# Kernel optimization log

Hardware: AMD Instinct MI355X
Metric: run time of the kernel (lower is better)

## Reference

```python
import jax, jax.numpy as jnp
import numpy as np

N_GRAPHS = 100
NODES_PER_GRAPH = 1000
N = N_GRAPHS * NODES_PER_GRAPH
DEG = 16
E = N * DEG
IN_FEATS = 64
HIDDEN = 128
READOUT_DIM = HIDDEN // 2
SLOPE = 0.01
EPS = 1e-5


def leaky(x):
    return jnp.where(x >= 0, x, SLOPE * x)


def _kaiming(k, shape):
    # torch kaiming_uniform_, fan_in mode, leaky_relu gain
    fan_in = shape[0]
    gain = np.sqrt(2.0 / (1.0 + SLOPE ** 2))
    bound = gain * np.sqrt(3.0 / fan_in)
    return jax.random.uniform(k, shape, jnp.float32, -bound, bound)


def setup_inputs() -> dict:
    key = jax.random.key(0)
    ks = jax.random.split(key, 16)
    node_feats = jax.random.normal(ks[0], (N, IN_FEATS), jnp.float32)
    # within-graph random edges (batched graph of equal-sized components)
    src_local = jax.random.randint(ks[1], (E,), 0, NODES_PER_GRAPH)
    dst_local = jax.random.randint(ks[2], (E,), 0, NODES_PER_GRAPH)
    edge_graph = jnp.repeat(jnp.arange(N_GRAPHS, dtype=jnp.int32), E // N_GRAPHS)
    src = (edge_graph * NODES_PER_GRAPH + src_local).astype(jnp.int32)
    dst = (edge_graph * NODES_PER_GRAPH + dst_local).astype(jnp.int32)
    edge_weights = jax.random.uniform(ks[3], (E,), jnp.float32)
    node_graph = jnp.repeat(jnp.arange(N_GRAPHS, dtype=jnp.int32), NODES_PER_GRAPH)
    return {
        "node_feats": node_feats,
        "edge_weights": edge_weights,
        "W1": _kaiming(ks[4], (IN_FEATS, HIDDEN)),
        "W2": _kaiming(ks[5], (HIDDEN, HIDDEN)),
        "gn1_alpha": jnp.ones((HIDDEN,), jnp.float32),
        "gn1_gamma": jnp.ones((HIDDEN,), jnp.float32),
        "gn1_beta": jnp.zeros((HIDDEN,), jnp.float32),
        "gn2_alpha": jnp.ones((HIDDEN,), jnp.float32),
        "gn2_gamma": jnp.ones((HIDDEN,), jnp.float32),
        "gn2_beta": jnp.zeros((HIDDEN,), jnp.float32),
        "r1_w1": _kaiming(ks[6], (HIDDEN, HIDDEN)),
        "r1_b1": jnp.zeros((HIDDEN,), jnp.float32),
        "r1_w2": _kaiming(ks[7], (HIDDEN, READOUT_DIM)),
        "r1_b2": jnp.zeros((READOUT_DIM,), jnp.float32),
        "r2_w1": _kaiming(ks[8], (HIDDEN, HIDDEN)),
        "r2_b1": jnp.zeros((HIDDEN,), jnp.float32),
        "r2_w2": _kaiming(ks[9], (HIDDEN, READOUT_DIM)),
        "r2_b2": jnp.zeros((READOUT_DIM,), jnp.float32),
        "src": src,
        "dst": dst,
        "node_graph": node_graph,
    }


def _graph_conv(x, W, src, dst, ew, out_isqrt, in_isqrt):
    # DGL GraphConv norm='both', no bias: D_in^{-1/2} A_w D_out^{-1/2} X W
    h = (x * out_isqrt[:, None]) @ W                 # [N, out]
    m = h[src] * ew[:, None]                         # [E, out] gather + edge weight
    agg = jax.ops.segment_sum(m, dst, num_segments=N)  # scatter-add
    return agg * in_isqrt[:, None]


def _graph_norm(x, alpha, gamma, beta, node_graph, inv_cnt):
    mean = jax.ops.segment_sum(x, node_graph, num_segments=N_GRAPHS) * inv_cnt
    sub = x - alpha * mean[node_graph]
    var = jax.ops.segment_sum(sub * sub, node_graph, num_segments=N_GRAPHS) * inv_cnt
    return gamma * sub / jnp.sqrt(var[node_graph] + EPS) + beta


def _readout(x, w1, b1, w2, b2, node_graph, inv_cnt):
    # deep-sets style universal readout: rho(mean(phi(h_v)))
    h = leaky(x @ w1 + b1)
    pooled = jax.ops.segment_sum(h, node_graph, num_segments=N_GRAPHS) * inv_cnt
    return leaky(pooled @ w2 + b2)


def reference(node_feats, edge_weights, W1, W2,
              gn1_alpha, gn1_gamma, gn1_beta,
              gn2_alpha, gn2_gamma, gn2_beta,
              r1_w1, r1_b1, r1_w2, r1_b2,
              r2_w1, r2_b1, r2_w2, r2_b2,
              src, dst, node_graph):
    ones_e = jnp.ones((E,), jnp.float32)
    out_deg = jnp.clip(jax.ops.segment_sum(ones_e, src, num_segments=N), 1.0)
    in_deg = jnp.clip(jax.ops.segment_sum(ones_e, dst, num_segments=N), 1.0)
    out_isqrt = jax.lax.rsqrt(out_deg)
    in_isqrt = jax.lax.rsqrt(in_deg)
    inv_cnt = 1.0 / NODES_PER_GRAPH

    h = _graph_conv(node_feats, W1, src, dst, edge_weights, out_isqrt, in_isqrt)
    h = leaky(_graph_norm(h, gn1_alpha, gn1_gamma, gn1_beta, node_graph, inv_cnt))
    # dropout is identity in eval mode
    r1 = _readout(h, r1_w1, r1_b1, r1_w2, r1_b2, node_graph, inv_cnt)
    m1 = jax.ops.segment_sum(h, node_graph, num_segments=N_GRAPHS) * inv_cnt

    h = _graph_conv(h, W2, src, dst, edge_weights, out_isqrt, in_isqrt)
    h = leaky(_graph_norm(h, gn2_alpha, gn2_gamma, gn2_beta, node_graph, inv_cnt))
    r2 = _readout(h, r2_w1, r2_b1, r2_w2, r2_b2, node_graph, inv_cnt)
    m2 = jax.ops.segment_sum(h, node_graph, num_segments=N_GRAPHS) * inv_cnt

    readout = jnp.concatenate([r1, m1, r2, m2], axis=1)  # [G, 2*H + 2*H/2] = [100, 384]
    return leaky(readout)
```

## Files before the change

### kernel.cpp

```cpp
#include <hip/hip_runtime.h>
#include <cstddef>
#include <cstdint>

#define NG   100
#define NPG  1000
#define NN   (NG * NPG)
#define NE   (NN * 16)
#define EPG  (NE / NG)
#define CSRG 20000
#define FIN  64
#define HID  128
#define RD   64
#define SLOPE 0.01f
#define EPSV  1e-5f
#define NSTRIP 250
#define GSN   40

using short8 = __attribute__((ext_vector_type(8))) short;
using f32x4  = __attribute__((ext_vector_type(4))) float;
typedef unsigned short u16;

__device__ __forceinline__ float leaky(float x) { return x >= 0.f ? x : SLOPE * x; }

__device__ __forceinline__ u16 f2bf(float f) {
  union { float f; unsigned u; } v; v.f = f;
  return (u16)((v.u + 0x7fffu + ((v.u >> 16) & 1u)) >> 16);
}
__device__ __forceinline__ float bf2f(u16 u) {
  union { unsigned u; float f; } v; v.u = ((unsigned)u) << 16;
  return v.f;
}

__device__ __forceinline__ bool swz(int b, int per_g, int& g, int& part) {
  const int xcd = b & 7;
  const int slot = b >> 3;
  g = xcd + 8 * (slot / per_g);
  part = slot % per_g;
  return g < NG;
}

__global__ __launch_bounds__(256) void wt_k(const float* __restrict__ W1,
                                            const float* __restrict__ W2,
                                            const float* __restrict__ R1,
                                            const float* __restrict__ R2,
                                            u16* __restrict__ Wt1,
                                            u16* __restrict__ Wt2,
                                            u16* __restrict__ Rt1,
                                            u16* __restrict__ Rt2) {
  const int idx = blockIdx.x * 256 + threadIdx.x;
  if (idx < FIN * HID) {
    const int n = idx >> 6, k = idx & 63;
    Wt1[idx] = f2bf(W1[k * HID + n]);
  } else {
    const int j = idx - FIN * HID;
    const int m = j >> 14, r = j & 16383;
    const int n = r >> 7, k = r & 127;
    const float* s = (m == 0) ? W2 : (m == 1) ? R1 : R2;
    u16* d = (m == 0) ? Wt2 : (m == 1) ? Rt1 : Rt2;
    d[r] = f2bf(s[k * HID + n]);
  }
}

__global__ __launch_bounds__(1024) void build_k(const int* __restrict__ src,
                                                const int* __restrict__ dst,
                                                const float* __restrict__ ew,
                                                int* __restrict__ cin_,
                                                int* __restrict__ cout_,
                                                int* __restrict__ offs,
                                                unsigned* __restrict__ csr) {
  __shared__ int hin[NPG];
  __shared__ int hout[NPG];
  __shared__ int cur[NPG];
  __shared__ int wtot[16];
  int g, part;
  if (!swz(blockIdx.x, 1, g, part)) return;
  const int t = threadIdx.x;
  const int lane = t & 63, wave = t >> 6;
  const int nb = g * NPG, eb = g * EPG;
  if (t < NPG) { hin[t] = 0; hout[t] = 0; }
  __syncthreads();
  for (int e = t; e < EPG; e += 1024) {
    atomicAdd(&hout[src[eb + e] - nb], 1);
    atomicAdd(&hin[dst[eb + e] - nb], 1);
  }
  __syncthreads();
  int v[4], vr[4];
  int loc = 0;
#pragma unroll
  for (int k = 0; k < 4; ++k) {
    const int idx = t * 4 + k;
    v[k] = (idx < NPG) ? hin[idx] : 0;
    vr[k] = (v[k] + 3) & ~3;
    loc += vr[k];
  }
  int incl = loc;
#pragma unroll
  for (int d = 1; d < 64; d <<= 1) {
    const int x = __shfl_up(incl, d);
    if (lane >= d) incl += x;
  }
  if (lane == 63) wtot[wave] = incl;
  if (t < NPG) { cin_[nb + t] = hin[t]; cout_[nb + t] = hout[t]; }
  __syncthreads();
  int wexc = 0;
  for (int i = 0; i < wave; ++i) wexc += wtot[i];
  int run = g * CSRG + wexc + (incl - loc);
#pragma unroll
  for (int k = 0; k < 4; ++k) {
    const int idx = t * 4 + k;
    if (idx < NPG) {
      offs[nb + idx] = run;
      cur[idx] = run;
      run += vr[k];
    }
  }
  __syncthreads();
  for (int e = t; e < EPG; e += 1024) {
    const int d = dst[eb + e] - nb;
    const int pos = atomicAdd(&cur[d], 1);
    csr[pos] = ((unsigned)(src[eb + e] - nb) << 16) | (unsigned)f2bf(ew[eb + e]);
  }
}

__global__ __launch_bounds__(256) void gemm1_k(const float* __restrict__ X,
                                               const u16* __restrict__ Wt,
                                               const int* __restrict__ cout_,
                                               u16* __restrict__ Y) {
  __shared__ u16 Xl[64 * FIN];
  __shared__ u16 Wl[HID * FIN];
  const int tid = threadIdx.x;
  const int wave = tid >> 6, lane = tid & 63, l15 = lane & 15, quad = lane >> 4;
  int g, part;
  if (!swz(blockIdx.x, 4, g, part)) return;
  const int base = g * NPG + part * NSTRIP;

  for (int i = tid; i < HID * (FIN / 8); i += 256) {
    const int n = i >> 3, c = i & 7;
    const short8 w = *(const short8*)(Wt + n * FIN + c * 8);
    *(short8*)&Wl[n * FIN + ((c ^ (n & 7)) << 3)] = w;
  }
  for (int pass = 0; pass < 4; ++pass) {
    __syncthreads();
    for (int i = tid; i < 64 * (FIN / 4); i += 256) {
      const int r = i >> 4;
      const int kq = i & 15;
      const int rowi = pass * 64 + r;
      ushort4 u = make_ushort4(0, 0, 0, 0);
      if (rowi < NSTRIP) {
        const float4 x = *(const float4*)(X + (size_t)(base + rowi) * FIN + kq * 4);
        u.x = f2bf(x.x); u.y = f2bf(x.y); u.z = f2bf(x.z); u.w = f2bf(x.w);
      }
      const int c = kq >> 1, half = kq & 1;
      *(ushort4*)&Xl[r * FIN + (((c ^ (r & 7)) << 3) | (half << 2))] = u;
    }
    __syncthreads();
    short8 a[2];
    const int arow = wave * 16 + l15;
#pragma unroll
    for (int kt = 0; kt < 2; ++kt)
      a[kt] = *(const short8*)&Xl[arow * FIN + (((kt * 4 + quad) ^ (l15 & 7)) << 3)];
    float sc[4];
    int rows[4];
#pragma unroll
    for (int r = 0; r < 4; ++r) {
      rows[r] = pass * 64 + wave * 16 + quad * 4 + r;
      sc[r] = (rows[r] < NSTRIP) ? rsqrtf(fmaxf((float)cout_[base + rows[r]], 1.0f)) : 0.f;
    }
#pragma unroll
    for (int ct = 0; ct < 8; ++ct) {
      f32x4 acc = {0.f, 0.f, 0.f, 0.f};
      const int brow = ct * 16 + l15;
#pragma unroll
      for (int kt = 0; kt < 2; ++kt) {
        const short8 b = *(const short8*)&Wl[brow * FIN + (((kt * 4 + quad) ^ (l15 & 7)) << 3)];
        acc = __builtin_amdgcn_mfma_f32_16x16x32_bf16(a[kt], b, acc, 0, 0, 0);
      }
      const int n = ct * 16 + l15;
#pragma unroll
      for (int r = 0; r < 4; ++r)
        if (rows[r] < NSTRIP) Y[(size_t)(base + rows[r]) * HID + n] = f2bf(acc[r] * sc[r]);
    }
  }
}

__global__ __launch_bounds__(256) void gemm_norm_k(const u16* __restrict__ Xb,
                                                   const u16* __restrict__ Wt,
                                                   const float* __restrict__ An,
                                                   const float* __restrict__ Bn,
                                                   const int* __restrict__ cout_,
                                                   u16* __restrict__ Y) {
  __shared__ u16 Xl[64 * HID];
  __shared__ u16 Wl[HID * HID];
  const int tid = threadIdx.x;
  const int wave = tid >> 6, lane = tid & 63, l15 = lane & 15, quad = lane >> 4;
  int g, part;
  if (!swz(blockIdx.x, 4, g, part)) return;
  const int base = g * NPG + part * NSTRIP;

  for (int i = tid; i < HID * (HID / 8); i += 256) {
    const int n = i >> 4, c = i & 15;
    const short8 w = *(const short8*)(Wt + n * HID + c * 8);
    *(short8*)&Wl[n * HID + ((c ^ (n & 15)) << 3)] = w;
  }
  for (int pass = 0; pass < 4; ++pass) {
    __syncthreads();
    for (int i = tid; i < 64 * 16; i += 256) {
      const int r = i >> 4;
      const int c8 = i & 15;
      const int rowi = pass * 64 + r;
      short8 o = {0, 0, 0, 0, 0, 0, 0, 0};
      if (rowi < NSTRIP) {
        const int node = base + rowi;
        const short8 xs = *(const short8*)(Xb + (size_t)node * HID + c8 * 8);
        const float4 Aa = *(const float4*)(An + (size_t)g * HID + c8 * 8);
        const float4 Ab = *(const float4*)(An + (size_t)g * HID + c8 * 8 + 4);
        const float4 Ba = *(const float4*)(Bn + (size_t)g * HID + c8 * 8);
        const float4 Bb = *(const float4*)(Bn + (size_t)g * HID + c8 * 8 + 4);
        const float Av[8] = {Aa.x, Aa.y, Aa.z, Aa.w, Ab.x, Ab.y, Ab.z, Ab.w};
        const float Bv[8] = {Ba.x, Ba.y, Ba.z, Ba.w, Bb.x, Bb.y, Bb.z, Bb.w};
#pragma unroll
        for (int j = 0; j < 8; ++j)
          o[j] = (short)f2bf(leaky(fmaf(Av[j], bf2f((u16)xs[j]), Bv[j])));
      }
      *(short8*)&Xl[r * HID + ((c8 ^ (r & 15)) << 3)] = o;
    }
    __syncthreads();
    short8 a[4];
    const int arow = wave * 16 + l15;
#pragma unroll
    for (int kt = 0; kt < 4; ++kt)
      a[kt] = *(const short8*)&Xl[arow * HID + (((kt * 4 + quad) ^ l15) << 3)];
    float sc[4];
    int rows[4];
#pragma unroll
    for (int r = 0; r < 4; ++r) {
      rows[r] = pass * 64 + wave * 16 + quad * 4 + r;
      sc[r] = (rows[r] < NSTRIP) ? rsqrtf(fmaxf((float)cout_[base + rows[r]], 1.0f)) : 0.f;
    }
#pragma unroll
    for (int ct = 0; ct < 8; ++ct) {
      f32x4 acc = {0.f, 0.f, 0.f, 0.f};
      const int brow = ct * 16 + l15;
#pragma unroll
      for (int kt = 0; kt < 4; ++kt) {
        const short8 b = *(const short8*)&Wl[brow * HID + (((kt * 4 + quad) ^ l15) << 3)];
        acc = __builtin_amdgcn_mfma_f32_16x16x32_bf16(a[kt], b, acc, 0, 0, 0);
      }
      const int n = ct * 16 + l15;
#pragma unroll
      for (int r = 0; r < 4; ++r)
        if (rows[r] < NSTRIP) Y[(size_t)(base + rows[r]) * HID + n] = f2bf(acc[r] * sc[r]);
    }
  }
}

__global__ __launch_bounds__(256) void phi_pool_k(const u16* __restrict__ Xb,
                                                  const float* __restrict__ An,
                                                  const float* __restrict__ Bn,
                                                  const u16* __restrict__ Wt,
                                                  const float* __restrict__ b1,
                                                  float* __restrict__ phi_sum,
                                                  float* __restrict__ h_sum) {
  __shared__ u16 Xl[64 * HID];
  __shared__ u16 Wl[HID * HID];
  __shared__ float red[16][HID];
  __shared__ float hred[16][HID];
  const int tid = threadIdx.x;
  const int wave = tid >> 6, lane = tid & 63, l15 = lane & 15, quad = lane >> 4;
  int g, part;
  if (!swz(blockIdx.x, 4, g, part)) return;
  const int base = g * NPG + part * NSTRIP;

  for (int i = tid; i < HID * (HID / 8); i += 256) {
    const int n = i >> 4, c = i & 15;
    const short8 w = *(const short8*)(Wt + n * HID + c * 8);
    *(short8*)&Wl[n * HID + ((c ^ (n & 15)) << 3)] = w;
  }
  float bcol[8];
#pragma unroll
  for (int ct = 0; ct < 8; ++ct) bcol[ct] = b1[ct * 16 + l15];

  float pooled[8] = {0.f, 0.f, 0.f, 0.f, 0.f, 0.f, 0.f, 0.f};
  float hp[8] = {0.f, 0.f, 0.f, 0.f, 0.f, 0.f, 0.f, 0.f};

  for (int pass = 0; pass < 4; ++pass) {
    __syncthreads();
    for (int i = tid; i < 64 * 16; i += 256) {
      const int r = i >> 4;
      const int c8 = i & 15;
      const int rowi = pass * 64 + r;
      short8 o = {0, 0, 0, 0, 0, 0, 0, 0};
      if (rowi < NSTRIP) {
        const int node = base + rowi;
        const short8 xs = *(const short8*)(Xb + (size_t)node * HID + c8 * 8);
        const float4 Aa = *(const float4*)(An + (size_t)g * HID + c8 * 8);
        const float4 Ab = *(const float4*)(An + (size_t)g * HID + c8 * 8 + 4);
        const float4 Ba = *(const float4*)(Bn + (size_t)g * HID + c8 * 8);
        const float4 Bb = *(const float4*)(Bn + (size_t)g * HID + c8 * 8 + 4);
        const float Av[8] = {Aa.x, Aa.y, Aa.z, Aa.w, Ab.x, Ab.y, Ab.z, Ab.w};
        const float Bv[8] = {Ba.x, Ba.y, Ba.z, Ba.w, Bb.x, Bb.y, Bb.z, Bb.w};
#pragma unroll
        for (int j = 0; j < 8; ++j) {
          const float xn = leaky(fmaf(Av[j], bf2f((u16)xs[j]), Bv[j]));
          hp[j] += xn;
          o[j] = (short)f2bf(xn);
        }
      }
      *(short8*)&Xl[r * HID + ((c8 ^ (r & 15)) << 3)] = o;
    }
    __syncthreads();
    short8 a[4];
    const int arow = wave * 16 + l15;
#pragma unroll
    for (int kt = 0; kt < 4; ++kt)
      a[kt] = *(const short8*)&Xl[arow * HID + (((kt * 4 + quad) ^ l15) << 3)];
#pragma unroll
    for (int ct = 0; ct < 8; ++ct) {
      f32x4 acc = {0.f, 0.f, 0.f, 0.f};
      const int brow = ct * 16 + l15;
#pragma unroll
      for (int kt = 0; kt < 4; ++kt) {
        const short8 b = *(const short8*)&Wl[brow * HID + (((kt * 4 + quad) ^ l15) << 3)];
        acc = __builtin_amdgcn_mfma_f32_16x16x32_bf16(a[kt], b, acc, 0, 0, 0);
      }
#pragma unroll
      for (int r = 0; r < 4; ++r) {
        const int rowi = pass * 64 + wave * 16 + quad * 4 + r;
        if (rowi < NSTRIP) pooled[ct] += leaky(acc[r] + bcol[ct]);
      }
    }
  }
  const int qi = wave * 4 + quad;
#pragma unroll
  for (int ct = 0; ct < 8; ++ct) red[qi][ct * 16 + l15] = pooled[ct];
#pragma unroll
  for (int j = 0; j < 8; ++j) hred[tid >> 4][(tid & 15) * 8 + j] = hp[j];
  __syncthreads();
  if (tid < HID) {
    float s = 0.f;
#pragma unroll
    for (int q = 0; q < 16; ++q) s += red[q][tid];
    unsafeAtomicAdd(&phi_sum[g * HID + tid], s);
  } else {
    const int t = tid - HID;
    float s = 0.f;
#pragma unroll
    for (int rr = 0; rr < 16; ++rr) s += hred[rr][t];
    unsafeAtomicAdd(&h_sum[g * HID + t], s);
  }
}

__global__ __launch_bounds__(256) void gather_k(const u16* __restrict__ H,
                                                const unsigned* __restrict__ csr,
                                                const int* __restrict__ offs,
                                                const int* __restrict__ cin_,
                                                u16* __restrict__ AGG,
                                                float* __restrict__ sx,
                                                float* __restrict__ sq) {
  __shared__ float redx[4][HID];
  __shared__ float redq[4][HID];
  const int wave = threadIdx.x >> 6;
  const int lane = threadIdx.x & 63;
  int g, part;
  if (!swz(blockIdx.x, 25, g, part)) return;
  const int nb = g * NPG;
  const int base = nb + part * GSN;
  const int loff = lane * 2;
  const u16* __restrict__ Hg = H + (size_t)nb * HID;

  float sxa = 0.f, sxb = 0.f, sqa = 0.f, sqb = 0.f;
  for (int i = 0; i < 5; ++i) {
    const int nA = base + wave + i * 4;
    const int nB = nA + GSN / 2;
    const int nuA = __builtin_amdgcn_readfirstlane(nA);
    const int nuB = __builtin_amdgcn_readfirstlane(nB);
    const int offA = __builtin_amdgcn_readfirstlane(offs[nuA]);
    const int cntA = __builtin_amdgcn_readfirstlane(cin_[nuA]);
    const int offB = __builtin_amdgcn_readfirstlane(offs[nuB]);
    const int cntB = __builtin_amdgcn_readfirstlane(cin_[nuB]);
    const float isqA = rsqrtf(fmaxf((float)cntA, 1.0f));
    const float isqB = rsqrtf(fmaxf((float)cntB, 1.0f));
    const uint4* __restrict__ pA =
        (const uint4*)__builtin_assume_aligned(csr + offA, 16);
    const uint4* __restrict__ pB =
        (const uint4*)__builtin_assume_aligned(csr + offB, 16);
    float axA = 0.f, ayA = 0.f, bxA = 0.f, byA = 0.f;
    float axB = 0.f, ayB = 0.f, bxB = 0.f, byB = 0.f;
    const int c4A = cntA >> 2, c4B = cntB >> 2;
    const int common = min(c4A, c4B);
    int t = 0;
    for (; t < common; ++t) {
      const uint4 rA = pA[t];
      const uint4 rB = pB[t];
      const unsigned a0 = *(const unsigned*)(Hg + (size_t)(rA.x >> 16) * HID + loff);
      const unsigned a1 = *(const unsigned*)(Hg + (size_t)(rA.y >> 16) * HID + loff);
      const unsigned a2 = *(const unsigned*)(Hg + (size_t)(rA.z >> 16) * HID + loff);
      const unsigned a3 = *(const unsigned*)(Hg + (size_t)(rA.w >> 16) * HID + loff);
      const unsigned b0 = *(const unsigned*)(Hg + (size_t)(rB.x >> 16) * HID + loff);
      const unsigned b1 = *(const unsigned*)(Hg + (size_t)(rB.y >> 16) * HID + loff);
      const unsigned b2 = *(const unsigned*)(Hg + (size_t)(rB.z >> 16) * HID + loff);
      const unsigned b3 = *(const unsigned*)(Hg + (size_t)(rB.w >> 16) * HID + loff);
      const float wA0 = bf2f((u16)(rA.x & 0xffffu));
      const float wA1 = bf2f((u16)(rA.y & 0xffffu));
      const float wA2 = bf2f((u16)(rA.z & 0xffffu));
      const float wA3 = bf2f((u16)(rA.w & 0xffffu));
      const float wB0 = bf2f((u16)(rB.x & 0xffffu));
      const float wB1 = bf2f((u16)(rB.y & 0xffffu));
      const float wB2 = bf2f((u16)(rB.z & 0xffffu));
      const float wB3 = bf2f((u16)(rB.w & 0xffffu));
      axA = fmaf(wA0, __uint_as_float(a0 << 16), axA);
      ayA = fmaf(wA0, __uint_as_float(a0 & 0xffff0000u), ayA);
      bxA = fmaf(wA1, __uint_as_float(a1 << 16), bxA);
      byA = fmaf(wA1, __uint_as_float(a1 & 0xffff0000u), byA);
      axA = fmaf(wA2, __uint_as_float(a2 << 16), axA);
      ayA = fmaf(wA2, __uint_as_float(a2 & 0xffff0000u), ayA);
      bxA = fmaf(wA3, __uint_as_float(a3 << 16), bxA);
      byA = fmaf(wA3, __uint_as_float(a3 & 0xffff0000u), byA);
      axB = fmaf(wB0, __uint_as_float(b0 << 16), axB);
      ayB = fmaf(wB0, __uint_as_float(b0 & 0xffff0000u), ayB);
      bxB = fmaf(wB1, __uint_as_float(b1 << 16), bxB);
      byB = fmaf(wB1, __uint_as_float(b1 & 0xffff0000u), byB);
      axB = fmaf(wB2, __uint_as_float(b2 << 16), axB);
      ayB = fmaf(wB2, __uint_as_float(b2 & 0xffff0000u), ayB);
      bxB = fmaf(wB3, __uint_as_float(b3 << 16), bxB);
      byB = fmaf(wB3, __uint_as_float(b3 & 0xffff0000u), byB);
    }
    for (int ta = t; ta < c4A; ++ta) {
      const uint4 rA = pA[ta];
      const unsigned a0 = *(const unsigned*)(Hg + (size_t)(rA.x >> 16) * HID + loff);
      const unsigned a1 = *(const unsigned*)(Hg + (size_t)(rA.y >> 16) * HID + loff);
      const unsigned a2 = *(const unsigned*)(Hg + (size_t)(rA.z >> 16) * HID + loff);
      const unsigned a3 = *(const unsigned*)(Hg + (size_t)(rA.w >> 16) * HID + loff);
      const float w0 = bf2f((u16)(rA.x & 0xffffu));
      const float w1 = bf2f((u16)(rA.y & 0xffffu));
      const float w2 = bf2f((u16)(rA.z & 0xffffu));
      const float w3 = bf2f((u16)(rA.w & 0xffffu));
      axA = fmaf(w0, __uint_as_float(a0 << 16), axA);
      ayA = fmaf(w0, __uint_as_float(a0 & 0xffff0000u), ayA);
      bxA = fmaf(w1, __uint_as_float(a1 << 16), bxA);
      byA = fmaf(w1, __uint_as_float(a1 & 0xffff0000u), byA);
      axA = fmaf(w2, __uint_as_float(a2 << 16), axA);
      ayA = fmaf(w2, __uint_as_float(a2 & 0xffff0000u), ayA);
      bxA = fmaf(w3, __uint_as_float(a3 << 16), bxA);
      byA = fmaf(w3, __uint_as_float(a3 & 0xffff0000u), byA);
    }
    for (int tb = t; tb < c4B; ++tb) {
      const uint4 rB = pB[tb];
      const unsigned b0 = *(const unsigned*)(Hg + (size_t)(rB.x >> 16) * HID + loff);
      const unsigned b1 = *(const unsigned*)(Hg + (size_t)(rB.y >> 16) * HID + loff);
      const unsigned b2 = *(const unsigned*)(Hg + (size_t)(rB.z >> 16) * HID + loff);
      const unsigned b3 = *(const unsigned*)(Hg + (size_t)(rB.w >> 16) * HID + loff);
      const float w0 = bf2f((u16)(rB.x & 0xffffu));
      const float w1 = bf2f((u16)(rB.y & 0xffffu));
      const float w2 = bf2f((u16)(rB.z & 0xffffu));
      const float w3 = bf2f((u16)(rB.w & 0xffffu));
      axB = fmaf(w0, __uint_as_float(b0 << 16), axB);
      ayB = fmaf(w0, __uint_as_float(b0 & 0xffff0000u), ayB);
      bxB = fmaf(w1, __uint_as_float(b1 << 16), bxB);
      byB = fmaf(w1, __uint_as_float(b1 & 0xffff0000u), byB);
      axB = fmaf(w2, __uint_as_float(b2 << 16), axB);
      ayB = fmaf(w2, __uint_as_float(b2 & 0xffff0000u), ayB);
      bxB = fmaf(w3, __uint_as_float(b3 << 16), bxB);
      byB = fmaf(w3, __uint_as_float(b3 & 0xffff0000u), byB);
    }
    for (int k = c4A << 2; k < cntA; ++k) {
      const unsigned r0 = csr[offA + k];
      const float w = bf2f((u16)(r0 & 0xffffu));
      const unsigned u0 = *(const unsigned*)(Hg + (size_t)(r0 >> 16) * HID + loff);
      axA = fmaf(w, __uint_as_float(u0 << 16), axA);
      ayA = fmaf(w, __uint_as_float(u0 & 0xffff0000u), ayA);
    }
    for (int k = c4B << 2; k < cntB; ++k) {
      const unsigned r0 = csr[offB + k];
      const float w = bf2f((u16)(r0 & 0xffffu));
      const unsigned u0 = *(const unsigned*)(Hg + (size_t)(r0 >> 16) * HID + loff);
      axB = fmaf(w, __uint_as_float(u0 << 16), axB);
      ayB = fmaf(w, __uint_as_float(u0 & 0xffff0000u), ayB);
    }
    const float rxA = (axA + bxA) * isqA;
    const float ryA = (ayA + byA) * isqA;
    const float rxB = (axB + bxB) * isqB;
    const float ryB = (ayB + byB) * isqB;
    *(unsigned*)(AGG + (size_t)nA * HID + loff) =
        (unsigned)f2bf(rxA) | ((unsigned)f2bf(ryA) << 16);
    *(unsigned*)(AGG + (size_t)nB * HID + loff) =
        (unsigned)f2bf(rxB) | ((unsigned)f2bf(ryB) << 16);
    sxa += rxA + rxB; sxb += ryA + ryB;
    sqa += rxA * rxA + rxB * rxB;
    sqb += ryA * ryA + ryB * ryB;
  }
  redx[wave][loff] = sxa; redx[wave][loff + 1] = sxb;
  redq[wave][loff] = sqa; redq[wave][loff + 1] = sqb;
  __syncthreads();
  const int tid = threadIdx.x;
  if (tid < HID) {
    unsafeAtomicAdd(&sx[g * HID + tid],
                    redx[0][tid] + redx[1][tid] + redx[2][tid] + redx[3][tid]);
  } else {
    const int t = tid - HID;
    unsafeAtomicAdd(&sq[g * HID + t],
                    redq[0][t] + redq[1][t] + redq[2][t] + redq[3][t]);
  }
}

__global__ __launch_bounds__(HID) void stats_k(const float* __restrict__ sx,
                                               const float* __restrict__ sq,
                                               const float* __restrict__ alpha,
                                               const float* __restrict__ gamma,
                                               const float* __restrict__ beta,
                                               float* __restrict__ An,
                                               float* __restrict__ Bn) {
  const int g = (blockIdx.x & 7) + 8 * (blockIdx.x >> 3);
  if (g >= NG) return;
  const int j = threadIdx.x;
  const float mean = sx[g * HID + j] * (1.0f / NPG);
  const float ex2 = sq[g * HID + j] * (1.0f / NPG);
  const float am = alpha[j] * mean;
  float var = ex2 - 2.0f * am * mean + am * am;
  var = fmaxf(var, 0.0f);
  const float rstd = rsqrtf(var + EPSV);
  const float A = gamma[j] * rstd;
  An[g * HID + j] = A;
  Bn[g * HID + j] = beta[j] - A * am;
}

__global__ __launch_bounds__(64) void finalize_k(const float* __restrict__ phi_sum,
                                                 const float* __restrict__ h_sum,
                                                 const float* __restrict__ w2,
                                                 const float* __restrict__ b2,
                                                 float* __restrict__ out,
                                                 int roff, int moff) {
  const int g = blockIdx.x;
  const int j = threadIdx.x;
  float acc = b2[j];
#pragma unroll 8
  for (int k = 0; k < HID; ++k)
    acc += (phi_sum[g * HID + k] * (1.0f / NPG)) * w2[k * RD + j];
  const float r = leaky(acc);
  out[g * 384 + roff + j] = leaky(r);
  out[g * 384 + moff + j] = leaky(h_sum[g * HID + j] * (1.0f / NPG));
  out[g * 384 + moff + 64 + j] = leaky(h_sum[g * HID + 64 + j] * (1.0f / NPG));
}

extern "C" void kernel_launch(void* const* d_in, const int* in_sizes, int n_in,
                              void* d_out, int out_size, void* d_ws, size_t ws_size,
                              hipStream_t stream) {
  const float* node_feats = (const float*)d_in[0];
  const float* ew   = (const float*)d_in[1];
  const float* W1   = (const float*)d_in[2];
  const float* W2   = (const float*)d_in[3];
  const float* g1a  = (const float*)d_in[4];
  const float* g1g  = (const float*)d_in[5];
  const float* g1b  = (const float*)d_in[6];
  const float* g2a  = (const float*)d_in[7];
  const float* g2g  = (const float*)d_in[8];
  const float* g2b  = (const float*)d_in[9];
  const float* r1w1 = (const float*)d_in[10];
  const float* r1b1 = (const float*)d_in[11];
  const float* r1w2 = (const float*)d_in[12];
  const float* r1b2 = (const float*)d_in[13];
  const float* r2w1 = (const float*)d_in[14];
  const float* r2b1 = (const float*)d_in[15];
  const float* r2w2 = (const float*)d_in[16];
  const float* r2b2 = (const float*)d_in[17];
  const int* src = (const int*)d_in[18];
  const int* dst = (const int*)d_in[19];
  float* out = (float*)d_out;

  char* wsb = (char*)d_ws;
  float* ps1     = (float*)wsb;
  float* hs1     = ps1 + NG * HID;
  float* ps2     = hs1 + NG * HID;
  float* hs2     = ps2 + NG * HID;
  float* sx1     = hs2 + NG * HID;
  float* sq1     = sx1 + NG * HID;
  float* sx2     = sq1 + NG * HID;
  float* sq2     = sx2 + NG * HID;
  int*   cin     = (int*)(sq2 + NG * HID);
  int*   cout_   = cin + NN;
  int*   offs    = cout_ + NN;
  unsigned* csr  = (unsigned*)(offs + NN);
  float* A1      = (float*)(csr + (size_t)NG * CSRG);
  float* B1      = A1 + NG * HID;
  float* A2      = B1 + NG * HID;
  float* B2      = A2 + NG * HID;
  u16*   Wt1     = (u16*)(B2 + NG * HID);
  u16*   Wt2     = Wt1 + HID * FIN;
  u16*   Rt1     = Wt2 + HID * HID;
  u16*   Rt2     = Rt1 + HID * HID;
  u16*   bufA    = Rt2 + HID * HID;
  u16*   bufB    = bufA + (size_t)NN * HID;

  hipMemsetAsync(d_ws, 0, (size_t)(8 * NG * HID) * sizeof(float), stream);

  wt_k<<<(FIN * HID + 3 * HID * HID) / 256, 256, 0, stream>>>(
      W1, W2, r1w1, r2w1, Wt1, Wt2, Rt1, Rt2);
  build_k<<<8 * 13, 1024, 0, stream>>>(src, dst, ew, cin, cout_, offs, csr);

  const int gemm_grid = 8 * 4 * 13;
  const int gather_grid = 8 * 25 * 13;
  const int stats_grid = 8 * 13;

  gemm1_k<<<gemm_grid, 256, 0, stream>>>(node_feats, Wt1, cout_, bufA);
  gather_k<<<gather_grid, 256, 0, stream>>>(bufA, csr, offs, cin, bufB, sx1, sq1);
  stats_k<<<stats_grid, HID, 0, stream>>>(sx1, sq1, g1a, g1g, g1b, A1, B1);
  phi_pool_k<<<gemm_grid, 256, 0, stream>>>(bufB, A1, B1, Rt1, r1b1, ps1, hs1);
  finalize_k<<<NG, 64, 0, stream>>>(ps1, hs1, r1w2, r1b2, out, 0, 64);

  gemm_norm_k<<<gemm_grid, 256, 0, stream>>>(bufB, Wt2, A1, B1, cout_, bufA);
  gather_k<<<gather_grid, 256, 0, stream>>>(bufA, csr, offs, cin, bufB, sx2, sq2);
  stats_k<<<stats_grid, HID, 0, stream>>>(sx2, sq2, g2a, g2g, g2b, A2, B2);
  phi_pool_k<<<gemm_grid, 256, 0, stream>>>(bufB, A2, B2, Rt2, r2b1, ps2, hs2);
  finalize_k<<<NG, 64, 0, stream>>>(ps2, hs2, r2w2, r2b2, out, 192, 256);
}
```

Baseline: 319.3 us.

## Prefetch next row tile into registers and batch edge loads in build

The three GEMM-style kernels now load the next 64-row tile of activations into registers right after the LDS barrier, so the global loads overlap the MFMA work of the current pass. The per-graph norm coefficients are hoisted out of the inner loop. The CSR build kernel batches four edge loads before issuing its shared atomics, which raises memory-level parallelism. phi_pool_k overlays its reduction buffers onto the X tile through a union to cut LDS use, adding an extra barrier and more register pressure.

```diff
diff --git a/kernel.cpp b/kernel.cpp
--- a/kernel.cpp
+++ b/kernel.cpp
@@ -79,9 +79,20 @@
   const int nb = g * NPG, eb = g * EPG;
   if (t < NPG) { hin[t] = 0; hout[t] = 0; }
   __syncthreads();
-  for (int e = t; e < EPG; e += 1024) {
-    atomicAdd(&hout[src[eb + e] - nb], 1);
-    atomicAdd(&hin[dst[eb + e] - nb], 1);
+  for (int e = t; e < EPG; e += 4096) {
+    int s4[4], d4[4];
+#pragma unroll
+    for (int k = 0; k < 4; ++k) {
+      const int ee = e + k * 1024;
+      if (ee < EPG) { s4[k] = src[eb + ee]; d4[k] = dst[eb + ee]; }
+      else d4[k] = -1;
+    }
+#pragma unroll
+    for (int k = 0; k < 4; ++k)
+      if (d4[k] >= 0) {
+        atomicAdd(&hout[s4[k] - nb], 1);
+        atomicAdd(&hin[d4[k] - nb], 1);
+      }
   }
   __syncthreads();
   int v[4], vr[4];
@@ -115,10 +126,20 @@
     }
   }
   __syncthreads();
-  for (int e = t; e < EPG; e += 1024) {
-    const int d = dst[eb + e] - nb;
-    const int pos = atomicAdd(&cur[d], 1);
-    csr[pos] = ((unsigned)(src[eb + e] - nb) << 16) | (unsigned)f2bf(ew[eb + e]);
+  for (int e = t; e < EPG; e += 4096) {
+    int s4[4], d4[4]; float w4[4];
+#pragma unroll
+    for (int k = 0; k < 4; ++k) {
+      const int ee = e + k * 1024;
+      if (ee < EPG) { s4[k] = src[eb + ee]; d4[k] = dst[eb + ee]; w4[k] = ew[eb + ee]; }
+      else d4[k] = -1;
+    }
+#pragma unroll
+    for (int k = 0; k < 4; ++k)
+      if (d4[k] >= 0) {
+        const int pos = atomicAdd(&cur[d4[k] - nb], 1);
+        csr[pos] = ((unsigned)(s4[k] - nb) << 16) | (unsigned)f2bf(w4[k]);
+      }
   }
 }
 
@@ -133,27 +154,40 @@
   int g, part;
   if (!swz(blockIdx.x, 4, g, part)) return;
   const int base = g * NPG + part * NSTRIP;
+  const int kq = tid & 15;
+  const int srow = tid >> 4;
 
   for (int i = tid; i < HID * (FIN / 8); i += 256) {
     const int n = i >> 3, c = i & 7;
     const short8 w = *(const short8*)(Wt + n * FIN + c * 8);
     *(short8*)&Wl[n * FIN + ((c ^ (n & 7)) << 3)] = w;
   }
+  float4 xpre[4];
+#pragma unroll
+  for (int it = 0; it < 4; ++it) {
+    const int rowi = srow + it * 16;
+    xpre[it] = (rowi < NSTRIP) ? *(const float4*)(X + (size_t)(base + rowi) * FIN + kq * 4)
+                               : make_float4(0.f, 0.f, 0.f, 0.f);
+  }
   for (int pass = 0; pass < 4; ++pass) {
     __syncthreads();
-    for (int i = tid; i < 64 * (FIN / 4); i += 256) {
-      const int r = i >> 4;
-      const int kq = i & 15;
-      const int rowi = pass * 64 + r;
-      ushort4 u = make_ushort4(0, 0, 0, 0);
-      if (rowi < NSTRIP) {
-        const float4 x = *(const float4*)(X + (size_t)(base + rowi) * FIN + kq * 4);
-        u.x = f2bf(x.x); u.y = f2bf(x.y); u.z = f2bf(x.z); u.w = f2bf(x.w);
-      }
+#pragma unroll
+    for (int it = 0; it < 4; ++it) {
+      const int r = srow + it * 16;
+      ushort4 u = make_ushort4(f2bf(xpre[it].x), f2bf(xpre[it].y),
+                               f2bf(xpre[it].z), f2bf(xpre[it].w));
       const int c = kq >> 1, half = kq & 1;
       *(ushort4*)&Xl[r * FIN + (((c ^ (r & 7)) << 3) | (half << 2))] = u;
     }
     __syncthreads();
+    if (pass < 3) {
+#pragma unroll
+      for (int it = 0; it < 4; ++it) {
+        const int rowi = (pass + 1) * 64 + srow + it * 16;
+        xpre[it] = (rowi < NSTRIP) ? *(const float4*)(X + (size_t)(base + rowi) * FIN + kq * 4)
+                                   : make_float4(0.f, 0.f, 0.f, 0.f);
+      }
+    }
     short8 a[2];
     const int arow = wave * 16 + l15;
 #pragma unroll
@@ -196,35 +230,54 @@
   int g, part;
   if (!swz(blockIdx.x, 4, g, part)) return;
   const int base = g * NPG + part * NSTRIP;
+  const int c8 = tid & 15;
+  const int srow = tid >> 4;
 
   for (int i = tid; i < HID * (HID / 8); i += 256) {
     const int n = i >> 4, c = i & 15;
     const short8 w = *(const short8*)(Wt + n * HID + c * 8);
     *(short8*)&Wl[n * HID + ((c ^ (n & 15)) << 3)] = w;
   }
+  float Av[8], Bv[8];
+  {
+    const float4 Aa = *(const float4*)(An + (size_t)g * HID + c8 * 8);
+    const float4 Ab = *(const float4*)(An + (size_t)g * HID + c8 * 8 + 4);
+    const float4 Ba = *(const float4*)(Bn + (size_t)g * HID + c8 * 8);
+    const float4 Bb = *(const float4*)(Bn + (size_t)g * HID + c8 * 8 + 4);
+    Av[0] = Aa.x; Av[1] = Aa.y; Av[2] = Aa.z; Av[3] = Aa.w;
+    Av[4] = Ab.x; Av[5] = Ab.y; Av[6] = Ab.z; Av[7] = Ab.w;
+    Bv[0] = Ba.x; Bv[1] = Ba.y; Bv[2] = Ba.z; Bv[3] = Ba.w;
+    Bv[4] = Bb.x; Bv[5] = Bb.y; Bv[6] = Bb.z; Bv[7] = Bb.w;
+  }
+  const short8 z8 = {0, 0, 0, 0, 0, 0, 0, 0};
+  short8 xpre[4];
+#pragma unroll
+  for (int it = 0; it < 4; ++it) {
+    const int rowi = srow + it * 16;
+    xpre[it] = (rowi < NSTRIP) ? *(const short8*)(Xb + (size_t)(base + rowi) * HID + c8 * 8) : z8;
+  }
   for (int pass = 0; pass < 4; ++pass) {
     __syncthreads();
-    for (int i = tid; i < 64 * 16; i += 256) {
-      const int r = i >> 4;
-      const int c8 = i & 15;
+#pragma unroll
+    for (int it = 0; it < 4; ++it) {
+      const int r = srow + it * 16;
       const int rowi = pass * 64 + r;
-      short8 o = {0, 0, 0, 0, 0, 0, 0, 0};
+      short8 o = z8;
       if (rowi < NSTRIP) {
-        const int node = base + rowi;
-        const short8 xs = *(const short8*)(Xb + (size_t)node * HID + c8 * 8);
-        const float4 Aa = *(const float4*)(An + (size_t)g * HID + c8 * 8);
-        const float4 Ab = *(const float4*)(An + (size_t)g * HID + c8 * 8 + 4);
-        const float4 Ba = *(const float4*)(Bn + (size_t)g * HID + c8 * 8);
-        const float4 Bb = *(const float4*)(Bn + (size_t)g * HID + c8 * 8 + 4);
-        const float Av[8] = {Aa.x, Aa.y, Aa.z, Aa.w, Ab.x, Ab.y, Ab.z, Ab.w};
-        const float Bv[8] = {Ba.x, Ba.y, Ba.z, Ba.w, Bb.x, Bb.y, Bb.z, Bb.w};
 #pragma unroll
         for (int j = 0; j < 8; ++j)
-          o[j] = (short)f2bf(leaky(fmaf(Av[j], bf2f((u16)xs[j]), Bv[j])));
+          o[j] = (short)f2bf(leaky(fmaf(Av[j], bf2f((u16)xpre[it][j]), Bv[j])));
       }
       *(short8*)&Xl[r * HID + ((c8 ^ (r & 15)) << 3)] = o;
     }
     __syncthreads();
+    if (pass < 3) {
+#pragma unroll
+      for (int it = 0; it < 4; ++it) {
+        const int rowi = (pass + 1) * 64 + srow + it * 16;
+        xpre[it] = (rowi < NSTRIP) ? *(const short8*)(Xb + (size_t)(base + rowi) * HID + c8 * 8) : z8;
+      }
+    }
     short8 a[4];
     const int arow = wave * 16 + l15;
 #pragma unroll
@@ -253,6 +306,9 @@
     }
   }
 }
+
+struct RedT { float red[16][HID]; float hred[16][HID]; };
+union ShT { u16 Xl[64 * HID]; RedT r; };
 
 __global__ __launch_bounds__(256) void phi_pool_k(const u16* __restrict__ Xb,
                                                   const float* __restrict__ An,
@@ -261,59 +317,75 @@
                                                   const float* __restrict__ b1,
                                                   float* __restrict__ phi_sum,
                                                   float* __restrict__ h_sum) {
-  __shared__ u16 Xl[64 * HID];
+  __shared__ ShT sh;
   __shared__ u16 Wl[HID * HID];
-  __shared__ float red[16][HID];
-  __shared__ float hred[16][HID];
   const int tid = threadIdx.x;
   const int wave = tid >> 6, lane = tid & 63, l15 = lane & 15, quad = lane >> 4;
   int g, part;
   if (!swz(blockIdx.x, 4, g, part)) return;
   const int base = g * NPG + part * NSTRIP;
+  const int c8 = tid & 15;
+  const int srow = tid >> 4;
 
   for (int i = tid; i < HID * (HID / 8); i += 256) {
     const int n = i >> 4, c = i & 15;
     const short8 w = *(const short8*)(Wt + n * HID + c * 8);
     *(short8*)&Wl[n * HID + ((c ^ (n & 15)) << 3)] = w;
   }
+  float Av[8], Bv[8];
+  {
+    const float4 Aa = *(const float4*)(An + (size_t)g * HID + c8 * 8);
+    const float4 Ab = *(const float4*)(An + (size_t)g * HID + c8 * 8 + 4);
+    const float4 Ba = *(const float4*)(Bn + (size_t)g * HID + c8 * 8);
+    const float4 Bb = *(const float4*)(Bn + (size_t)g * HID + c8 * 8 + 4);
+    Av[0] = Aa.x; Av[1] = Aa.y; Av[2] = Aa.z; Av[3] = Aa.w;
+    Av[4] = Ab.x; Av[5] = Ab.y; Av[6] = Ab.z; Av[7] = Ab.w;
+    Bv[0] = Ba.x; Bv[1] = Ba.y; Bv[2] = Ba.z; Bv[3] = Ba.w;
+    Bv[4] = Bb.x; Bv[5] = Bb.y; Bv[6] = Bb.z; Bv[7] = Bb.w;
+  }
   float bcol[8];
 #pragma unroll
   for (int ct = 0; ct < 8; ++ct) bcol[ct] = b1[ct * 16 + l15];
 
   float pooled[8] = {0.f, 0.f, 0.f, 0.f, 0.f, 0.f, 0.f, 0.f};
   float hp[8] = {0.f, 0.f, 0.f, 0.f, 0.f, 0.f, 0.f, 0.f};
-
+  const short8 z8 = {0, 0, 0, 0, 0, 0, 0, 0};
+  short8 xpre[4];
+#pragma unroll
+  for (int it = 0; it < 4; ++it) {
+    const int rowi = srow + it * 16;
+    xpre[it] = (rowi < NSTRIP) ? *(const short8*)(Xb + (size_t)(base + rowi) * HID + c8 * 8) : z8;
+  }
   for (int pass = 0; pass < 4; ++pass) {
     __syncthreads();
-    for (int i = tid; i < 64 * 16; i += 256) {
-      const int r = i >> 4;
-      const int c8 = i & 15;
+#pragma unroll
+    for (int it = 0; it < 4; ++it) {
+      const int r = srow + it * 16;
       const int rowi = pass * 64 + r;
-      short8 o = {0, 0, 0, 0, 0, 0, 0, 0};
+      short8 o = z8;
       if (rowi < NSTRIP) {
-        const int node = base + rowi;
-        const short8 xs = *(const short8*)(Xb + (size_t)node * HID + c8 * 8);
-        const float4 Aa = *(const float4*)(An + (size_t)g * HID + c8 * 8);
-        const float4 Ab = *(const float4*)(An + (size_t)g * HID + c8 * 8 + 4);
-        const float4 Ba = *(const float4*)(Bn + (size_t)g * HID + c8 * 8);
-        const float4 Bb = *(const float4*)(Bn + (size_t)g * HID + c8 * 8 + 4);
-        const float Av[8] = {Aa.x, Aa.y, Aa.z, Aa.w, Ab.x, Ab.y, Ab.z, Ab.w};
-        const float Bv[8] = {Ba.x, Ba.y, Ba.z, Ba.w, Bb.x, Bb.y, Bb.z, Bb.w};
 #pragma unroll
         for (int j = 0; j < 8; ++j) {
-          const float xn = leaky(fmaf(Av[j], bf2f((u16)xs[j]), Bv[j]));
+          const float xn = leaky(fmaf(Av[j], bf2f((u16)xpre[it][j]), Bv[j]));
           hp[j] += xn;
           o[j] = (short)f2bf(xn);
         }
       }
-      *(short8*)&Xl[r * HID + ((c8 ^ (r & 15)) << 3)] = o;
+      *(short8*)&sh.Xl[r * HID + ((c8 ^ (r & 15)) << 3)] = o;
     }
     __syncthreads();
+    if (pass < 3) {
+#pragma unroll
+      for (int it = 0; it < 4; ++it) {
+        const int rowi = (pass + 1) * 64 + srow + it * 16;
+        xpre[it] = (rowi < NSTRIP) ? *(const short8*)(Xb + (size_t)(base + rowi) * HID + c8 * 8) : z8;
+      }
+    }
     short8 a[4];
     const int arow = wave * 16 + l15;
 #pragma unroll
     for (int kt = 0; kt < 4; ++kt)
-      a[kt] = *(const short8*)&Xl[arow * HID + (((kt * 4 + quad) ^ l15) << 3)];
+      a[kt] = *(const short8*)&sh.Xl[arow * HID + (((kt * 4 + quad) ^ l15) << 3)];
 #pragma unroll
     for (int ct = 0; ct < 8; ++ct) {
       f32x4 acc = {0.f, 0.f, 0.f, 0.f};
@@ -330,22 +402,23 @@
       }
     }
   }
+  __syncthreads();
   const int qi = wave * 4 + quad;
 #pragma unroll
-  for (int ct = 0; ct < 8; ++ct) red[qi][ct * 16 + l15] = pooled[ct];
-#pragma unroll
-  for (int j = 0; j < 8; ++j) hred[tid >> 4][(tid & 15) * 8 + j] = hp[j];
+  for (int ct = 0; ct < 8; ++ct) sh.r.red[qi][ct * 16 + l15] = pooled[ct];
+#pragma unroll
+  for (int j = 0; j < 8; ++j) sh.r.hred[tid >> 4][(tid & 15) * 8 + j] = hp[j];
   __syncthreads();
   if (tid < HID) {
     float s = 0.f;
 #pragma unroll
-    for (int q = 0; q < 16; ++q) s += red[q][tid];
+    for (int q = 0; q < 16; ++q) s += sh.r.red[q][tid];
     unsafeAtomicAdd(&phi_sum[g * HID + tid], s);
   } else {
     const int t = tid - HID;
     float s = 0.f;
 #pragma unroll
-    for (int rr = 0; rr < 16; ++rr) s += hred[rr][t];
+    for (int rr = 0; rr < 16; ++rr) s += sh.r.hred[rr][t];
     unsafeAtomicAdd(&h_sum[g * HID + t], s);
   }
 }
```

Measured after the change: 297.2 us. -6.9%, faster.
